# Kernel tuning notes

Measured on AMD Instinct MI355X. Metric: run time of the kernel, lower is better.

Reference implementation:

```python
import jax, jax.numpy as jnp
import numpy as np


def setup_inputs() -> dict:
    key = jax.random.key(0)
    k1, k2, k3 = jax.random.split(key, 3)
    B, H, S, D = 4, 16, 1024, 64
    return {
        "query": jax.random.normal(k1, (B, H, S, D), dtype=jnp.float32),
        "key": jax.random.normal(k2, (B, H, D, S), dtype=jnp.float32),  # pre-transposed K
        "scale_factor": 8,  # sqrt(head_dim)
        "attention_mask": jnp.zeros((S, S), dtype=jnp.float32),
        "value": jax.random.normal(k3, (B, H, S, D), dtype=jnp.float32),
    }


def reference(query, key, scale_factor, attention_mask, value):
    # Batched equivalent of the per-(b,h) Python loop:
    # scores = Q @ K^T / scale + mask; probs = softmax(scores); out = probs @ V
    scores = jnp.matmul(query, key) / scale_factor  # [B,H,S,S]
    if attention_mask is not None:
        scores = scores + attention_mask  # broadcast [S,S] over [B,H,S,S]
    probs = jax.nn.softmax(scores, axis=-1)
    return jnp.matmul(probs, value)  # [B,H,S,D]
```

## Files before the change

### kernel.cpp

```cpp
#include <hip/hip_runtime.h>

#define BH  64
#define SEQ 1024
#define DIM 64
#define KT  64

typedef __attribute__((ext_vector_type(8))) short  short8;
typedef __attribute__((ext_vector_type(4))) float  floatx4;

__device__ __forceinline__ ushort f2bf(float x) {
    union { float f; uint u; } v; v.f = x;
    uint r = v.u + 0x7FFFu + ((v.u >> 16) & 1u);
    return (ushort)(r >> 16);
}
__device__ __forceinline__ uint pack2(float lo, float hi) {
    return (uint)f2bf(lo) | ((uint)f2bf(hi) << 16);
}
__device__ __forceinline__ void gld_lds16(const void* g, void* l) {
    __builtin_amdgcn_global_load_lds(
        (const __attribute__((address_space(1))) unsigned int*)g,
        (__attribute__((address_space(3))) unsigned int*)l, 16, 0, 0);
}


__global__ __launch_bounds__(256) void prep_kv_kernel(
    const float* __restrict__ Kg, const float* __restrict__ Vg,
    ushort* __restrict__ Kbf, ushort* __restrict__ Vbf)
{
    __shared__ float tile[32][33];
    const int zz = blockIdx.z;
    const int tx = threadIdx.x & 31, ty = threadIdx.x >> 5;
    if (zz < BH) {
        const int c0 = blockIdx.x * 32;
        const int r0 = blockIdx.y * 32;
        const float* ip = Kg + (size_t)zz * DIM * SEQ;
        char* op = (char*)(Kbf + (size_t)zz * SEQ * DIM);
#pragma unroll
        for (int i = 0; i < 4; ++i)
            tile[ty + 8 * i][tx] = ip[(size_t)(r0 + ty + 8 * i) * SEQ + c0 + tx];
        __syncthreads();
#pragma unroll
        for (int i = 0; i < 4; ++i) {
            const int s = c0 + ty + 8 * i, d = r0 + tx;
            *(ushort*)(op + (size_t)s * 128 + (((d >> 3) ^ (s & 7)) * 16) + (d & 7) * 2)
                = f2bf(tile[tx][ty + 8 * i]);
        }
    } else {
        const int head = zz - BH;
        const int r0 = blockIdx.x * 32;
        const int c0 = blockIdx.y * 32;
        const float* ip = Vg + (size_t)head * SEQ * DIM;
        char* op = (char*)(Vbf + (size_t)head * SEQ * DIM);
#pragma unroll
        for (int i = 0; i < 4; ++i)
            tile[ty + 8 * i][tx] = ip[(size_t)(r0 + ty + 8 * i) * DIM + c0 + tx];
        __syncthreads();
#pragma unroll
        for (int i = 0; i < 4; ++i) {
            const int d = c0 + ty + 8 * i, s = r0 + tx;
            *(ushort*)(op + (size_t)(s >> 6) * 8192 + (size_t)d * 128
                          + ((((s & 63) >> 3) ^ (d & 7)) * 16) + (s & 7) * 2)
                = f2bf(tile[tx][ty + 8 * i]);
        }
    }
}

__global__ __launch_bounds__(256, 4) void mha_mfma4_kernel(
    const float*  __restrict__ Q,
    const ushort* __restrict__ Kbf,
    const int*    __restrict__ scale_p,
    const float*  __restrict__ mask,
    const ushort* __restrict__ Vbf,
    float*        __restrict__ O)
{
    __shared__ __align__(16) char smem[40960];

    const int t    = threadIdx.x;
    const int lane = t & 63, w = t >> 6;
    const int li   = lane & 15, quad = lane >> 4, lx = li & 7;
    const int bh   = blockIdx.x & 63;
    const int q0   = (blockIdx.x >> 6) * 64;

    const float inv_scale = 1.0f / (float)scale_p[0];
    char* Ps  = smem + 32768;
    char* psw = Ps + w * 2048;

    {
        const float* Qg = Q + ((size_t)bh * SEQ + q0) * DIM;
        const int rr = t >> 4, cc = (t & 15) * 4;
#pragma unroll
        for (int i = 0; i < 4; ++i) {
            const int row = rr + 16 * i;
            float4 v = *(const float4*)(Qg + (size_t)row * DIM + cc);
            uint2 pw; pw.x = pack2(v.x, v.y); pw.y = pack2(v.z, v.w);
            *(uint2*)(Ps + row * 128 + (((cc >> 3) ^ (row & 7)) * 16) + (cc & 7) * 2) = pw;
        }
    }
    __syncthreads();
    const short8 qa0 = *(const short8*)(psw + li * 128 + ((quad ^ lx) * 16));
    const short8 qa1 = *(const short8*)(psw + li * 128 + (((4 + quad) ^ lx) * 16));

    floatx4 o[4] = {floatx4{0,0,0,0}, floatx4{0,0,0,0},
                    floatx4{0,0,0,0}, floatx4{0,0,0,0}};
    float l_r[4] = {0.f, 0.f, 0.f, 0.f};

    const char* KgH = (const char*)(Kbf + (size_t)bh * SEQ * DIM);
    const char* VgH = (const char*)(Vbf + (size_t)bh * SEQ * DIM);
    const int   so  = w * 2048 + lane * 16;
    const float* mrow = mask + (size_t)(q0 + w * 16 + quad * 4) * SEQ + li;

    {
        char* ksd = smem + w * 2048;
        char* vtd = smem + 8192 + w * 2048;
        gld_lds16(KgH + so,        ksd);
        gld_lds16(KgH + so + 1024, ksd + 1024);
        gld_lds16(VgH + so,        vtd);
        gld_lds16(VgH + so + 1024, vtd + 1024);
    }
    __syncthreads();

    for (int kt = 0; kt < SEQ / KT; ++kt) {
        const int cur = kt & 1;
        const char* Ks = smem + cur * 16384;
        const char* Vt = Ks + 8192;
        const int key0 = kt * KT;

        float mv[16];
#pragma unroll
        for (int n = 0; n < 4; ++n)
#pragma unroll
            for (int r = 0; r < 4; ++r)
                mv[n * 4 + r] = mrow[(size_t)r * SEQ + key0 + n * 16];

        if (kt < SEQ / KT - 1) {
            const int nb = cur ^ 1;
            const char* kg = KgH + (kt + 1) * 8192 + so;
            const char* vg = VgH + (kt + 1) * 8192 + so;
            char* ksd = smem + nb * 16384 + w * 2048;
            char* vtd = smem + nb * 16384 + 8192 + w * 2048;
            gld_lds16(kg,        ksd);
            gld_lds16(kg + 1024, ksd + 1024);
            gld_lds16(vg,        vtd);
            gld_lds16(vg + 1024, vtd + 1024);
        }

        floatx4 c[4] = {floatx4{0,0,0,0}, floatx4{0,0,0,0},
                        floatx4{0,0,0,0}, floatx4{0,0,0,0}};
#pragma unroll
        for (int n = 0; n < 4; ++n) {
            const char* krow = Ks + (n * 16 + li) * 128;
            short8 b0 = *(const short8*)(krow + ((quad ^ lx) * 16));
            short8 b1 = *(const short8*)(krow + (((4 + quad) ^ lx) * 16));
            c[n] = __builtin_amdgcn_mfma_f32_16x16x32_bf16(qa0, b0, c[n], 0, 0, 0);
            c[n] = __builtin_amdgcn_mfma_f32_16x16x32_bf16(qa1, b1, c[n], 0, 0, 0);
        }

#pragma unroll
        for (int n = 0; n < 4; ++n)
#pragma unroll
            for (int r = 0; r < 4; ++r) {
                float s = fminf(fmaf(c[n][r], inv_scale, mv[n * 4 + r]), 80.f);
                float p = __expf(s);
                l_r[r] += p;
                const int row = quad * 4 + r, col = n * 16 + li;
                *(ushort*)(psw + row * 128 + (((col >> 3) ^ (row & 7)) * 16)
                           + (col & 7) * 2) = f2bf(p);
            }

#pragma unroll
        for (int kk = 0; kk < 2; ++kk) {
            short8 a = *(const short8*)(psw + li * 128 + (((kk * 4 + quad) ^ lx) * 16));
#pragma unroll
            for (int n = 0; n < 4; ++n) {
                const char* vrow = Vt + (n * 16 + li) * 128;
                short8 b = *(const short8*)(vrow + (((kk * 4 + quad) ^ lx) * 16));
                o[n] = __builtin_amdgcn_mfma_f32_16x16x32_bf16(a, b, o[n], 0, 0, 0);
            }
        }

        __syncthreads();
    }

#pragma unroll
    for (int off = 1; off < 16; off <<= 1)
#pragma unroll
        for (int r = 0; r < 4; ++r)
            l_r[r] += __shfl_xor(l_r[r], off);

    float* Og = O + ((size_t)bh * SEQ + q0) * DIM;
#pragma unroll
    for (int r = 0; r < 4; ++r) {
        const float inv_l = 1.0f / l_r[r];
#pragma unroll
        for (int n = 0; n < 4; ++n)
            Og[(size_t)(w * 16 + quad * 4 + r) * DIM + n * 16 + li] = o[n][r] * inv_l;
    }
}

extern "C" void kernel_launch(void* const* d_in, const int* in_sizes, int n_in,
                              void* d_out, int out_size, void* d_ws, size_t ws_size,
                              hipStream_t stream) {
    const float* Q     = (const float*)d_in[0];
    const float* K     = (const float*)d_in[1];
    const int*   scale = (const int*)d_in[2];
    const float* mask  = (const float*)d_in[3];
    const float* V     = (const float*)d_in[4];
    float*       Out   = (float*)d_out;

    ushort* Kbf = (ushort*)d_ws;
    ushort* Vbf = Kbf + (size_t)BH * SEQ * DIM;

    prep_kv_kernel<<<dim3(SEQ / 32, DIM / 32, 2 * BH), 256, 0, stream>>>(K, V, Kbf, Vbf);
    mha_mfma4_kernel<<<dim3(BH * (SEQ / KT)), 256, 0, stream>>>(Q, Kbf, scale, mask, Vbf, Out);
}
```

Before: 141.2 us.

## Keep softmax probabilities in registers via transposed QK MFMA and lane swaps

Swaps the MFMA operand order so the score tile comes out transposed. Each lane then holds the bf16 probabilities for one query row. A permlane/shuffle exchange builds the P operand for the PV MFMA directly in registers, which removes the per-wave LDS round trip for P and cuts shared memory from 40 KB to 32 KB. The mask is read as float4 along the row, and the row sum becomes a single accumulator over the bf16-rounded values, reduced with two shuffles. The cost is extra cross-lane permute instructions, plus a dependence on the permlane swap builtins being available, with a shuffle fallback otherwise.

```diff
diff --git a/kernel.cpp b/kernel.cpp
--- a/kernel.cpp
+++ b/kernel.cpp
@@ -7,12 +7,17 @@
 
 typedef __attribute__((ext_vector_type(8))) short  short8;
 typedef __attribute__((ext_vector_type(4))) float  floatx4;
+typedef __attribute__((ext_vector_type(2))) unsigned int uint2v;
 
 __device__ __forceinline__ ushort f2bf(float x) {
     union { float f; uint u; } v; v.f = x;
     uint r = v.u + 0x7FFFu + ((v.u >> 16) & 1u);
     return (ushort)(r >> 16);
 }
+__device__ __forceinline__ float bf2f(ushort b) {
+    union { uint u; float f; } v; v.u = ((uint)b) << 16;
+    return v.f;
+}
 __device__ __forceinline__ uint pack2(float lo, float hi) {
     return (uint)f2bf(lo) | ((uint)f2bf(hi) << 16);
 }
@@ -20,6 +25,33 @@
     __builtin_amdgcn_global_load_lds(
         (const __attribute__((address_space(1))) unsigned int*)g,
         (__attribute__((address_space(3))) unsigned int*)l, 16, 0, 0);
+}
+
+#if defined(__has_builtin)
+#if __has_builtin(__builtin_amdgcn_permlane32_swap) && __has_builtin(__builtin_amdgcn_permlane16_swap)
+#define HAVE_PERMLANE_SWAP 1
+#endif
+#endif
+
+__device__ __forceinline__ void quad_exchange(uint& A0, uint& A1, uint& B0, uint& B1,
+                                              int lane) {
+#ifdef HAVE_PERMLANE_SWAP
+    uint2v s;
+    s = __builtin_amdgcn_permlane32_swap(A0, B0, false, false); A0 = s.x; B0 = s.y;
+    s = __builtin_amdgcn_permlane16_swap(A0, B0, false, false); A0 = s.x; B0 = s.y;
+    s = __builtin_amdgcn_permlane32_swap(A1, B1, false, false); A1 = s.x; B1 = s.y;
+    s = __builtin_amdgcn_permlane16_swap(A1, B1, false, false); A1 = s.x; B1 = s.y;
+#else
+    const bool hi5 = (lane & 32) != 0, hi4 = (lane & 16) != 0;
+    uint t0 = (uint)__shfl_xor((int)A0, 32), u0 = (uint)__shfl_xor((int)B0, 32);
+    uint nA0 = hi5 ? u0 : A0, nB0 = hi5 ? B0 : t0;
+    uint t1 = (uint)__shfl_xor((int)A1, 32), u1 = (uint)__shfl_xor((int)B1, 32);
+    uint nA1 = hi5 ? u1 : A1, nB1 = hi5 ? B1 : t1;
+    uint v0 = (uint)__shfl_xor((int)nA0, 16), w0 = (uint)__shfl_xor((int)nB0, 16);
+    A0 = hi4 ? w0 : nA0; B0 = hi4 ? nB0 : v0;
+    uint v1 = (uint)__shfl_xor((int)nA1, 16), w1 = (uint)__shfl_xor((int)nB1, 16);
+    A1 = hi4 ? w1 : nA1; B1 = hi4 ? nB1 : v1;
+#endif
 }
 
 
@@ -65,7 +97,7 @@
     }
 }
 
-__global__ __launch_bounds__(256, 4) void mha_mfma4_kernel(
+__global__ __launch_bounds__(256, 4) void mha_mfma5_kernel(
     const float*  __restrict__ Q,
     const ushort* __restrict__ Kbf,
     const int*    __restrict__ scale_p,
@@ -73,7 +105,7 @@
     const ushort* __restrict__ Vbf,
     float*        __restrict__ O)
 {
-    __shared__ __align__(16) char smem[40960];
+    __shared__ __align__(16) char smem[32768];
 
     const int t    = threadIdx.x;
     const int lane = t & 63, w = t >> 6;
@@ -82,9 +114,8 @@
     const int q0   = (blockIdx.x >> 6) * 64;
 
     const float inv_scale = 1.0f / (float)scale_p[0];
-    char* Ps  = smem + 32768;
-    char* psw = Ps + w * 2048;
-
+
+    char* Qs = smem + 16384;
     {
         const float* Qg = Q + ((size_t)bh * SEQ + q0) * DIM;
         const int rr = t >> 4, cc = (t & 15) * 4;
@@ -93,30 +124,27 @@
             const int row = rr + 16 * i;
             float4 v = *(const float4*)(Qg + (size_t)row * DIM + cc);
             uint2 pw; pw.x = pack2(v.x, v.y); pw.y = pack2(v.z, v.w);
-            *(uint2*)(Ps + row * 128 + (((cc >> 3) ^ (row & 7)) * 16) + (cc & 7) * 2) = pw;
+            *(uint2*)(Qs + row * 128 + (((cc >> 3) ^ (row & 7)) * 16) + (cc & 7) * 2) = pw;
         }
     }
     __syncthreads();
-    const short8 qa0 = *(const short8*)(psw + li * 128 + ((quad ^ lx) * 16));
-    const short8 qa1 = *(const short8*)(psw + li * 128 + (((4 + quad) ^ lx) * 16));
+    const char* qrow = Qs + (w * 16 + li) * 128;
+    const short8 qa0 = *(const short8*)(qrow + ((quad ^ lx) * 16));
+    const short8 qa1 = *(const short8*)(qrow + (((4 + quad) ^ lx) * 16));
 
     floatx4 o[4] = {floatx4{0,0,0,0}, floatx4{0,0,0,0},
                     floatx4{0,0,0,0}, floatx4{0,0,0,0}};
-    float l_r[4] = {0.f, 0.f, 0.f, 0.f};
+    float l_acc = 0.f;
 
     const char* KgH = (const char*)(Kbf + (size_t)bh * SEQ * DIM);
     const char* VgH = (const char*)(Vbf + (size_t)bh * SEQ * DIM);
     const int   so  = w * 2048 + lane * 16;
-    const float* mrow = mask + (size_t)(q0 + w * 16 + quad * 4) * SEQ + li;
-
-    {
-        char* ksd = smem + w * 2048;
-        char* vtd = smem + 8192 + w * 2048;
-        gld_lds16(KgH + so,        ksd);
-        gld_lds16(KgH + so + 1024, ksd + 1024);
-        gld_lds16(VgH + so,        vtd);
-        gld_lds16(VgH + so + 1024, vtd + 1024);
-    }
+    const float* mrow = mask + (size_t)(q0 + w * 16 + li) * SEQ + quad * 4;
+
+    gld_lds16(KgH + so,               smem + w * 2048);
+    gld_lds16(KgH + so + 1024,        smem + w * 2048 + 1024);
+    gld_lds16(VgH + so,               smem + 8192 + w * 2048);
+    gld_lds16(VgH + so + 1024,        smem + 8192 + w * 2048 + 1024);
     __syncthreads();
 
     for (int kt = 0; kt < SEQ / KT; ++kt) {
@@ -125,23 +153,19 @@
         const char* Vt = Ks + 8192;
         const int key0 = kt * KT;
 
-        float mv[16];
+        float4 mv[4];
 #pragma unroll
         for (int n = 0; n < 4; ++n)
-#pragma unroll
-            for (int r = 0; r < 4; ++r)
-                mv[n * 4 + r] = mrow[(size_t)r * SEQ + key0 + n * 16];
+            mv[n] = *(const float4*)(mrow + key0 + n * 16);
 
         if (kt < SEQ / KT - 1) {
             const int nb = cur ^ 1;
             const char* kg = KgH + (kt + 1) * 8192 + so;
             const char* vg = VgH + (kt + 1) * 8192 + so;
-            char* ksd = smem + nb * 16384 + w * 2048;
-            char* vtd = smem + nb * 16384 + 8192 + w * 2048;
-            gld_lds16(kg,        ksd);
-            gld_lds16(kg + 1024, ksd + 1024);
-            gld_lds16(vg,        vtd);
-            gld_lds16(vg + 1024, vtd + 1024);
+            gld_lds16(kg,        smem + nb * 16384 + w * 2048);
+            gld_lds16(kg + 1024, smem + nb * 16384 + w * 2048 + 1024);
+            gld_lds16(vg,        smem + nb * 16384 + 8192 + w * 2048);
+            gld_lds16(vg + 1024, smem + nb * 16384 + 8192 + w * 2048 + 1024);
         }
 
         floatx4 c[4] = {floatx4{0,0,0,0}, floatx4{0,0,0,0},
@@ -151,46 +175,49 @@
             const char* krow = Ks + (n * 16 + li) * 128;
             short8 b0 = *(const short8*)(krow + ((quad ^ lx) * 16));
             short8 b1 = *(const short8*)(krow + (((4 + quad) ^ lx) * 16));
-            c[n] = __builtin_amdgcn_mfma_f32_16x16x32_bf16(qa0, b0, c[n], 0, 0, 0);
-            c[n] = __builtin_amdgcn_mfma_f32_16x16x32_bf16(qa1, b1, c[n], 0, 0, 0);
-        }
-
-#pragma unroll
-        for (int n = 0; n < 4; ++n)
+            c[n] = __builtin_amdgcn_mfma_f32_16x16x32_bf16(b0, qa0, c[n], 0, 0, 0);
+            c[n] = __builtin_amdgcn_mfma_f32_16x16x32_bf16(b1, qa1, c[n], 0, 0, 0);
+        }
+
+        uint px[4][2];
+#pragma unroll
+        for (int n = 0; n < 4; ++n) {
+            ushort h[4];
 #pragma unroll
             for (int r = 0; r < 4; ++r) {
-                float s = fminf(fmaf(c[n][r], inv_scale, mv[n * 4 + r]), 80.f);
-                float p = __expf(s);
-                l_r[r] += p;
-                const int row = quad * 4 + r, col = n * 16 + li;
-                *(ushort*)(psw + row * 128 + (((col >> 3) ^ (row & 7)) * 16)
-                           + (col & 7) * 2) = f2bf(p);
+                float s = fminf(fmaf(c[n][r], inv_scale, (&mv[n].x)[r]), 80.f);
+                h[r] = f2bf(__expf(s));
+                l_acc += bf2f(h[r]);
             }
+            px[n][0] = (uint)h[0] | ((uint)h[1] << 16);
+            px[n][1] = (uint)h[2] | ((uint)h[3] << 16);
+        }
 
 #pragma unroll
         for (int kk = 0; kk < 2; ++kk) {
-            short8 a = *(const short8*)(psw + li * 128 + (((kk * 4 + quad) ^ lx) * 16));
+            uint A0 = px[2 * kk][0],     A1 = px[2 * kk][1];
+            uint B0 = px[2 * kk + 1][0], B1 = px[2 * kk + 1][1];
+            quad_exchange(A0, A1, B0, B1, lane);
+            union { uint u[4]; short8 s; } af;
+            af.u[0] = A0; af.u[1] = A1; af.u[2] = B0; af.u[3] = B1;
 #pragma unroll
             for (int n = 0; n < 4; ++n) {
                 const char* vrow = Vt + (n * 16 + li) * 128;
                 short8 b = *(const short8*)(vrow + (((kk * 4 + quad) ^ lx) * 16));
-                o[n] = __builtin_amdgcn_mfma_f32_16x16x32_bf16(a, b, o[n], 0, 0, 0);
+                o[n] = __builtin_amdgcn_mfma_f32_16x16x32_bf16(af.s, b, o[n], 0, 0, 0);
             }
         }
 
         __syncthreads();
     }
 
-#pragma unroll
-    for (int off = 1; off < 16; off <<= 1)
-#pragma unroll
-        for (int r = 0; r < 4; ++r)
-            l_r[r] += __shfl_xor(l_r[r], off);
+    l_acc += __shfl_xor(l_acc, 16);
+    l_acc += __shfl_xor(l_acc, 32);
 
     float* Og = O + ((size_t)bh * SEQ + q0) * DIM;
 #pragma unroll
     for (int r = 0; r < 4; ++r) {
-        const float inv_l = 1.0f / l_r[r];
+        const float inv_l = 1.0f / __shfl(l_acc, quad * 4 + r);
 #pragma unroll
         for (int n = 0; n < 4; ++n)
             Og[(size_t)(w * 16 + quad * 4 + r) * DIM + n * 16 + li] = o[n][r] * inv_l;
@@ -211,5 +238,5 @@
     ushort* Vbf = Kbf + (size_t)BH * SEQ * DIM;
 
     prep_kv_kernel<<<dim3(SEQ / 32, DIM / 32, 2 * BH), 256, 0, stream>>>(K, V, Kbf, Vbf);
-    mha_mfma4_kernel<<<dim3(BH * (SEQ / KT)), 256, 0, stream>>>(Q, Kbf, scale, mask, Vbf, Out);
-}
+    mha_mfma5_kernel<<<dim3(BH * (SEQ / KT)), 256, 0, stream>>>(Q, Kbf, scale, mask, Vbf, Out);
+}
```

Result: slower. 146.4 us (+3.6%).
